# Performance work log

Hardware: AMD Instinct MI355X
Metric: run time of the kernel (lower is better)

The kernel has to match this reference:

```python
import jax, jax.numpy as jnp
import numpy as np
from jax import lax


def linear_recurrence(decays, impulses):
    """s[t] = decays[t]*s[t-1] + impulses[t], s[-1]=0, via associative scan over axis 0."""
    def comb(e1, e2):
        a1, b1 = e1
        a2, b2 = e2
        return a2 * a1, a2 * b1 + b2
    return lax.associative_scan(comb, (decays, impulses), axis=0)[1]


def setup_inputs() -> dict:
    key = jax.random.key(0)
    ks = jax.random.split(key, 6)
    b, T, d = 16, 1024, 128
    n, m, k = 64, 128, 16
    x = jax.random.normal(ks[0], (b, T, d), jnp.float32)
    R = jax.random.normal(ks[1], (d, k), jnp.float32)               # fixed projection
    theta = jax.random.uniform(ks[2], (k, n // 2), jnp.float32, -np.pi, np.pi)  # eig angles
    C = jax.random.uniform(ks[3], (k, m, n), jnp.float32, -1e-6, 1e-6) / n
    D = jax.random.uniform(ks[4], (k, m), jnp.float32, -1e-3, 1e-3)
    Do = jax.random.uniform(ks[5], (m,), jnp.float32, -1e-7, 1e-7)
    return {"x": x, "R": R, "theta": theta, "C": C, "D": D, "Do": Do}


def _ldstack(x, R, theta, C, D, Do, Delta=2, standard=True):
    c64 = jnp.complex64
    b, T, d = x.shape
    k, half = theta.shape
    n = 2 * half
    m = C.shape[1]
    # (b,T,d) -> (T,b,d) complex, project d -> k
    xc = jnp.transpose(x, (1, 0, 2)).astype(c64) @ R.astype(c64)  # (T,b,k)
    # unitary eigenvalues: lnλ = i*[θ, -θ]
    lnlam = (1j * jnp.concatenate([theta, -theta], axis=1)).astype(c64)  # (k,n)
    lam = jnp.exp(lnlam)
    # B' coefficients (log-space product over eigenvalue ratios, diag excluded)
    eye = jnp.eye(n, dtype=bool)
    ratios = jnp.where(eye[None], 0.0, lam[:, :, None] / lam[:, None, :])  # (k,n,n)
    B = jnp.exp(-jnp.sum(jnp.log(1.0 - ratios), axis=1))                    # (k,n)
    # C' coefficients: C'[k,j,m] = sum_i C[k,m,i] * λ[k,j]^{-(n-i)}
    powers = (n - jnp.arange(1, n + 1)).astype(c64)           # (n,) = [n-1,...,0]
    U = jnp.exp(-powers[None, :, None] * lnlam[:, None, :])   # (k,i,j)
    Cp = jnp.einsum('kmi,kij->kjm', C.astype(c64), U)         # (k,n,m)
    Dc = D.astype(c64)
    Doc = Do.astype(c64)

    alpha = None
    y = None
    for _ in range(Delta):
        Bx = (xc[..., None] * B).reshape(T, b, k * n)          # (T,b,k*n)
        if alpha is None:
            al = jnp.broadcast_to(lam.reshape(1, 1, k * n), (T, b, k * n))
        else:
            al = (alpha * lam).reshape(T, b, k * n)
        if standard:
            z = jnp.zeros((1, b, k * n), c64)
            al = jnp.concatenate([z, al[:-1]], axis=0)
            Bx = jnp.concatenate([z, Bx[:-1]], axis=0)
        s = linear_recurrence(al, Bx).reshape(T, b, k, n)      # (T,b,k,n)
        y = (jnp.einsum('tbkn,knm->tbkm', s, Cp)
             + xc[..., None] * Dc[None, None]
             + Doc)                                            # (T,b,k,m)
        ls = lam[None, None] * s
        alpha = (1.0 / jnp.sqrt(1.0 + jnp.abs(ls) ** 2)).astype(c64)  # recipsq
    y = jnp.mean(y, axis=2).real                               # (T,b,m)
    return jnp.transpose(y, (1, 0, 2))                         # (b,T,m)


def reference(x, R, theta, C, D, Do):
    return _ldstack(x, R, theta, C, D, Do, Delta=2, standard=True)
```

## Files before the change

### kernel.cpp

```cpp
#include <hip/hip_runtime.h>
#include <math.h>

#define TLEN 1024
#define BSZ  16
#define DIN  128
#define KP   16
#define NEIG 64
#define MOUT 128
#define CHUNK_T 256
#define NCHUNK  4

static constexpr size_t XCQ_OFF = 0;
static constexpr size_t LAM_OFF = 262144;
static constexpr size_t BQ_OFF  = 264192;
static constexpr size_t CP_OFF  = 266240;
static constexpr size_t ST_OFF  = 528384;
static constexpr size_t S2_OFF  = 593920;
static constexpr size_t P_OFF   = 8982528;

__device__ __forceinline__ float f32cos(float x) { return (float)cos((double)x); }
__device__ __forceinline__ float f32sin(float x) { return (float)sin((double)x); }

__device__ __forceinline__ float2 cdiv32(float ar, float ai, float cr, float ci) {
  float2 o;
  if (fabsf(ci) <= fabsf(cr)) {
    float rat = __fdiv_rn(ci, cr);
    float scl = __fdiv_rn(1.0f, __fadd_rn(cr, __fmul_rn(ci, rat)));
    o.x = __fmul_rn(__fadd_rn(ar, __fmul_rn(ai, rat)), scl);
    o.y = __fmul_rn(__fsub_rn(ai, __fmul_rn(ar, rat)), scl);
  } else {
    float rat = __fdiv_rn(cr, ci);
    float scl = __fdiv_rn(1.0f, __fadd_rn(ci, __fmul_rn(cr, rat)));
    o.x = __fmul_rn(__fadd_rn(__fmul_rn(ar, rat), ai), scl);
    o.y = __fmul_rn(__fsub_rn(__fmul_rn(ai, rat), ar), scl);
  }
  return o;
}

__global__ __launch_bounds__(256) void k_lam_B(const float* __restrict__ theta,
                        float2* __restrict__ lam, float2* __restrict__ Bq) {
  __shared__ float2 terms[4][64];
  int wid  = threadIdx.x >> 6;
  int lane = threadIdx.x & 63;
  int idx = blockIdx.x * 4 + wid;
  int k = idx >> 6, j = idx & 63;
  float thj = (j < 32) ? theta[k * 32 + j] : -theta[k * 32 + (j - 32)];
  float ljr = f32cos(thj), lji = f32sin(thj);
  float2 tm = make_float2(0.f, 0.f);
  if (lane != j) {
    int i = lane;
    float thi = (i < 32) ? theta[k * 32 + i] : -theta[k * 32 + (i - 32)];
    float lir = f32cos(thi), lii = f32sin(thi);
    float2 r = cdiv32(lir, lii, ljr, lji);
    float tr = __fsub_rn(1.0f, r.x);
    float ti = __fsub_rn(0.0f, r.y);
    double h = sqrt((double)tr * tr + (double)ti * ti);
    tm.x = (float)log(h);
    tm.y = (float)atan2((double)ti, (double)tr);
  }
  terms[wid][lane] = tm;
  __syncthreads();
  if (lane == 0) {
    lam[idx] = make_float2(ljr, lji);
    float sr = 0.f, si = 0.f;
    for (int i = 0; i < NEIG; ++i) {
      sr = __fadd_rn(sr, terms[wid][i].x);
      si = __fadd_rn(si, terms[wid][i].y);
    }
    float er = (float)exp((double)(-sr));
    float cc = f32cos(-si), ss = f32sin(-si);
    Bq[idx] = make_float2(__fmul_rn(er, cc), __fmul_rn(er, ss));
  }
}

__global__ __launch_bounds__(128) void k_Cp(const float* __restrict__ theta,
                     const float* __restrict__ C, float2* __restrict__ Cp) {
  __shared__ float2 sU[64];
  __shared__ float  sC[128][65];
  int tid = threadIdx.x;
  int kj = blockIdx.x;
  int j = kj & 63, k = kj >> 6;
  float lnim = (j < 32) ? theta[k * 32 + j] : -theta[k * 32 + (j - 32)];
  if (tid < 64) {
    int i = tid;
    float p = (float)(63 - i);
    float ph = -__fmul_rn(p, lnim);
    sU[i] = make_float2(f32cos(ph), f32sin(ph));
  }
  const float* Ck = C + ((size_t)k << 13);
  for (int e = tid; e < 128 * 64; e += 128) {
    sC[e >> 6][e & 63] = Ck[e];
  }
  __syncthreads();
  int m = tid;
  float ar = 0.f, ai = 0.f;
  #pragma unroll 8
  for (int i = 0; i < NEIG; ++i) {
    float Cv = sC[m][i];
    float2 U = sU[i];
    ar = __fadd_rn(ar, __fmul_rn(Cv, U.x));
    ai = __fadd_rn(ai, __fmul_rn(Cv, U.y));
  }
  Cp[(size_t)(k * 64 + j) * MOUT + m] = make_float2(ar, ai);
}

__global__ __launch_bounds__(256) void k_xc(const float* __restrict__ x,
                     const float* __restrict__ R, float* __restrict__ xcq) {
  __shared__ float sX[16][132];
  __shared__ float sR[128][16];
  int tid = threadIdx.x;
  int rBase = blockIdx.x * 16;
  for (int e = tid; e < DIN * KP; e += 256) sR[e >> 4][e & 15] = R[e];
  #pragma unroll
  for (int it = 0; it < 2; ++it) {
    int e = tid + it * 256;
    int row = e >> 5, q = e & 31;
    int g = rBase + row;
    int t = g >> 4, b = g & 15;
    float4 v = *(const float4*)(x + ((size_t)b * TLEN + t) * DIN + q * 4);
    *(float4*)&sX[row][q * 4] = v;
  }
  __syncthreads();
  int r = tid >> 4, k = tid & 15;
  double acc = 0.0;
  #pragma unroll 16
  for (int d = 0; d < DIN; ++d)
    acc = fma((double)sX[r][d], (double)sR[d][k], acc);
  xcq[(size_t)(rBase + r) * KP + k] = (float)acc;
}

__global__ __launch_bounds__(64) void k_scan(const float2* __restrict__ lam,
                        const float2* __restrict__ Bq,
                        const float* __restrict__ xcq,
                        float2* __restrict__ S2,
                        float* __restrict__ state, int c) {
  __shared__ float sXq[CHUNK_T];
  int j = threadIdx.x;
  int chain = blockIdx.x;
  int b = chain >> 4, k = chain & 15;
  int mode = k * 64 + j;
  int t0 = c * CHUNK_T;
  int tlBeg = (c == 0) ? 1 : 0;
  for (int i = j; i < CHUNK_T; i += 64) {
    int g = t0 + tlBeg - 1 + i;
    sXq[i] = xcq[(size_t)g * (BSZ * KP) + b * KP + k];
  }
  __syncthreads();
  float lr = lam[mode].x, li = lam[mode].y;
  float Br = Bq[mode].x,  Bi = Bq[mode].y;
  float* st = state + (size_t)(chain * 64 + j) * 4;
  float s1r, s1i, s2r, s2i;
  if (c == 0) { s1r = s1i = s2r = s2i = 0.f; }
  else        { s1r = st[0]; s1i = st[1]; s2r = st[2]; s2i = st[3]; }
  if (c == 0)
    S2[(size_t)(0 * BSZ + b) * 1024 + mode] = make_float2(s2r, s2i);

  int tl = tlBeg;
  for (; tl + 8 <= CHUNK_T; tl += 8) {
    float als[8];
    #pragma unroll
    for (int u = 0; u < 8; ++u) {
      float xq = sXq[tl - tlBeg + u];
      float lsr = __fsub_rn(__fmul_rn(lr, s1r), __fmul_rn(li, s1i));
      float lsi = __fadd_rn(__fmul_rn(lr, s1i), __fmul_rn(li, s1r));
      float h  = (float)sqrt((double)lsr * lsr + (double)lsi * lsi);
      als[u] = __fdiv_rn(1.0f, __fsqrt_rn(__fadd_rn(1.0f, __fmul_rn(h, h))));
      float bxr = __fmul_rn(xq, Br), bxi = __fmul_rn(xq, Bi);
      s1r = __fadd_rn(lsr, bxr);
      s1i = __fadd_rn(lsi, bxi);
    }
    #pragma unroll
    for (int u = 0; u < 8; ++u) {
      float xq = sXq[tl - tlBeg + u];
      float al = als[u];
      float bxr = __fmul_rn(xq, Br), bxi = __fmul_rn(xq, Bi);
      float a2r = __fmul_rn(al, lr), a2i = __fmul_rn(al, li);
      float t2r = __fsub_rn(__fmul_rn(a2r, s2r), __fmul_rn(a2i, s2i));
      float t2i = __fadd_rn(__fmul_rn(a2r, s2i), __fmul_rn(a2i, s2r));
      s2r = __fadd_rn(t2r, bxr);
      s2i = __fadd_rn(t2i, bxi);
      S2[(size_t)((tl + u) * BSZ + b) * 1024 + mode] = make_float2(s2r, s2i);
    }
  }
  for (; tl < CHUNK_T; ++tl) {
    float xq = sXq[tl - tlBeg];
    float lsr = __fsub_rn(__fmul_rn(lr, s1r), __fmul_rn(li, s1i));
    float lsi = __fadd_rn(__fmul_rn(lr, s1i), __fmul_rn(li, s1r));
    float h  = (float)sqrt((double)lsr * lsr + (double)lsi * lsi);
    float al = __fdiv_rn(1.0f, __fsqrt_rn(__fadd_rn(1.0f, __fmul_rn(h, h))));
    float bxr = __fmul_rn(xq, Br), bxi = __fmul_rn(xq, Bi);
    float a2r = __fmul_rn(al, lr), a2i = __fmul_rn(al, li);
    float t2r = __fsub_rn(__fmul_rn(a2r, s2r), __fmul_rn(a2i, s2i));
    float t2i = __fadd_rn(__fmul_rn(a2r, s2i), __fmul_rn(a2i, s2r));
    s2r = __fadd_rn(t2r, bxr);
    s2i = __fadd_rn(t2i, bxi);
    s1r = __fadd_rn(lsr, bxr);
    s1i = __fadd_rn(lsi, bxi);
    S2[(size_t)(tl * BSZ + b) * 1024 + mode] = make_float2(s2r, s2i);
  }
  st[0] = s1r; st[1] = s1i; st[2] = s2r; st[3] = s2i;
}

__global__ __launch_bounds__(256) void k_y(const float2* __restrict__ S2,
                     const float2* __restrict__ Cp, const float* __restrict__ xcq,
                     const float* __restrict__ D, const float* __restrict__ Dov,
                     float* __restrict__ P, int c) {
  __shared__ float2 sS2t[16][129];
  __shared__ float2 sCp[16][128];
  int tid = threadIdx.x;
  int kidx = blockIdx.x >> 5;
  int rt   = blockIdx.x & 31;
  int rowBase = rt * 128;
  int rg = tid & 15;
  int cg = tid >> 4;
  int c0 = cg * 8;
  float acc[8][8];
  #pragma unroll
  for (int jj = 0; jj < 8; ++jj)
    #pragma unroll
    for (int q = 0; q < 8; ++q) acc[jj][q] = 0.f;

  int a_n2[4], a_row[4], w_n[4], w_col2[4];
  #pragma unroll
  for (int it = 0; it < 4; ++it) {
    int e = tid + it * 256;
    a_n2[it] = (e & 7) * 2;  a_row[it] = e >> 3;
    w_n[it] = e >> 6;        w_col2[it] = (e & 63) * 2;
  }

  float4 regA[4], regB[4];
  #pragma unroll
  for (int it = 0; it < 4; ++it) {
    regA[it] = *(const float4*)(S2 + (size_t)(rowBase + a_row[it]) * 1024
                                   + kidx * 64 + a_n2[it]);
    regB[it] = *(const float4*)(Cp + (size_t)(kidx * 64 + w_n[it]) * MOUT + w_col2[it]);
  }

  #pragma unroll 1
  for (int nh = 0; nh < 4; ++nh) {
    __syncthreads();
    #pragma unroll
    for (int it = 0; it < 4; ++it) {
      sS2t[a_n2[it]][a_row[it]]     = make_float2(regA[it].x, regA[it].y);
      sS2t[a_n2[it] + 1][a_row[it]] = make_float2(regA[it].z, regA[it].w);
      *(float4*)&sCp[w_n[it]][w_col2[it]] = regB[it];
    }
    __syncthreads();
    if (nh < 3) {
      #pragma unroll
      for (int it = 0; it < 4; ++it) {
        regA[it] = *(const float4*)(S2 + (size_t)(rowBase + a_row[it]) * 1024
                                       + kidx * 64 + (nh + 1) * 16 + a_n2[it]);
        regB[it] = *(const float4*)(Cp + (size_t)(kidx * 64 + (nh + 1) * 16 + w_n[it]) * MOUT
                                       + w_col2[it]);
      }
    }
    #pragma unroll 4
    for (int n = 0; n < 16; ++n) {
      float2 a[8];
      #pragma unroll
      for (int jj = 0; jj < 8; ++jj) a[jj] = sS2t[n][rg + jj * 16];
      float4 w[4];
      #pragma unroll
      for (int q = 0; q < 4; ++q) w[q] = *(const float4*)&sCp[n][c0 + q * 2];
      float cx[8] = {w[0].x, w[0].z, w[1].x, w[1].z, w[2].x, w[2].z, w[3].x, w[3].z};
      float cy[8] = {w[0].y, w[0].w, w[1].y, w[1].w, w[2].y, w[2].w, w[3].y, w[3].w};
      #pragma unroll
      for (int jj = 0; jj < 8; ++jj)
        #pragma unroll
        for (int q = 0; q < 8; ++q)
          acc[jj][q] = __fadd_rn(acc[jj][q],
              __fsub_rn(__fmul_rn(a[jj].x, cx[q]), __fmul_rn(a[jj].y, cy[q])));
    }
  }
  float dv[8], ovv[8];
  *(float4*)&dv[0]  = *(const float4*)(D + kidx * MOUT + c0);
  *(float4*)&dv[4]  = *(const float4*)(D + kidx * MOUT + c0 + 4);
  *(float4*)&ovv[0] = *(const float4*)(Dov + c0);
  *(float4*)&ovv[4] = *(const float4*)(Dov + c0 + 4);
  #pragma unroll
  for (int jj = 0; jj < 8; ++jj) {
    int row = rowBase + rg + jj * 16;
    float xv = xcq[(size_t)(c * 4096 + row) * KP + kidx];
    float res[8];
    #pragma unroll
    for (int q = 0; q < 8; ++q)
      res[q] = __fadd_rn(__fadd_rn(acc[jj][q], __fmul_rn(xv, dv[q])), ovv[q]);
    float* pp = P + ((size_t)kidx * 4096 + row) * MOUT + c0;
    *(float4*)pp       = make_float4(res[0], res[1], res[2], res[3]);
    *(float4*)(pp + 4) = make_float4(res[4], res[5], res[6], res[7]);
  }
}

__global__ __launch_bounds__(256) void k_combine(const float* __restrict__ P,
                     float* __restrict__ out, int c) {
  int idx = blockIdx.x * 256 + threadIdx.x;
  int r  = idx >> 5;
  int m4 = (idx & 31) * 4;
  float4 s = *(const float4*)(P + (size_t)r * MOUT + m4);
  #pragma unroll
  for (int k = 1; k < KP; ++k) {
    float4 p = *(const float4*)(P + ((size_t)k * 4096 + r) * MOUT + m4);
    s.x = __fadd_rn(s.x, p.x);
    s.y = __fadd_rn(s.y, p.y);
    s.z = __fadd_rn(s.z, p.z);
    s.w = __fadd_rn(s.w, p.w);
  }
  int rg = c * 4096 + r;
  int t = rg >> 4, b = rg & 15;
  float4 res;
  res.x = __fdiv_rn(s.x, 16.0f);
  res.y = __fdiv_rn(s.y, 16.0f);
  res.z = __fdiv_rn(s.z, 16.0f);
  res.w = __fdiv_rn(s.w, 16.0f);
  *(float4*)(out + ((size_t)b * TLEN + t) * MOUT + m4) = res;
}

extern "C" void kernel_launch(void* const* d_in, const int* in_sizes, int n_in,
                              void* d_out, int out_size, void* d_ws, size_t ws_size,
                              hipStream_t stream) {
  const float* x     = (const float*)d_in[0];
  const float* R     = (const float*)d_in[1];
  const float* theta = (const float*)d_in[2];
  const float* C     = (const float*)d_in[3];
  const float* D     = (const float*)d_in[4];
  const float* Do    = (const float*)d_in[5];
  float* out = (float*)d_out;
  float* ws  = (float*)d_ws;
  float*  xcq = ws + XCQ_OFF;
  float2* lam = (float2*)(ws + LAM_OFF);
  float2* Bq  = (float2*)(ws + BQ_OFF);
  float2* Cp  = (float2*)(ws + CP_OFF);
  float*  st  = ws + ST_OFF;
  float2* S2  = (float2*)(ws + S2_OFF);
  float*  P   = ws + P_OFF;

  hipLaunchKernelGGL(k_lam_B, dim3(256),  dim3(256), 0, stream, theta, lam, Bq);
  hipLaunchKernelGGL(k_Cp,    dim3(1024), dim3(128), 0, stream, theta, C, Cp);
  hipLaunchKernelGGL(k_xc,    dim3(1024), dim3(256), 0, stream, x, R, xcq);
  for (int c = 0; c < NCHUNK; ++c) {
    hipLaunchKernelGGL(k_scan,    dim3(256), dim3(64),  0, stream, lam, Bq, xcq, S2, st, c);
    hipLaunchKernelGGL(k_y,       dim3(512), dim3(256), 0, stream, S2, Cp, xcq, D, Do, P, c);
    hipLaunchKernelGGL(k_combine, dim3(512), dim3(256), 0, stream, P, out, c);
  }
}
```

Baseline: 396.3 us.

## Halve k_y row tile to 64 and drop register prefetch to double block count

The k_y tile shrinks from 128 to 64 rows per block, so the grid doubles to 1024 blocks and each thread holds a 4x8 accumulator instead of 8x8. The register double-buffered prefetch of S2 and Cp tiles is removed in favour of direct global-to-shared loads inside the loop, and shared-memory padding is adjusted. The goal is more parallelism and occupancy on the device. In exchange, each loaded Cp tile is reused across fewer rows and global load latency is no longer overlapped with compute.

After: 372.1 us. -6.1%, faster.

```diff
diff --git a/kernel.cpp b/kernel.cpp
--- a/kernel.cpp
+++ b/kernel.cpp
@@ -205,68 +205,55 @@
                      const float2* __restrict__ Cp, const float* __restrict__ xcq,
                      const float* __restrict__ D, const float* __restrict__ Dov,
                      float* __restrict__ P, int c) {
-  __shared__ float2 sS2t[16][129];
-  __shared__ float2 sCp[16][128];
+  __shared__ float2 sS2t[16][65];
+  __shared__ float2 sCp[16][130];
   int tid = threadIdx.x;
-  int kidx = blockIdx.x >> 5;
-  int rt   = blockIdx.x & 31;
-  int rowBase = rt * 128;
+  int kidx = blockIdx.x >> 6;
+  int rt   = blockIdx.x & 63;
+  int rowBase = rt * 64;
   int rg = tid & 15;
   int cg = tid >> 4;
   int c0 = cg * 8;
-  float acc[8][8];
+  float acc[4][8];
   #pragma unroll
-  for (int jj = 0; jj < 8; ++jj)
+  for (int jj = 0; jj < 4; ++jj)
     #pragma unroll
     for (int q = 0; q < 8; ++q) acc[jj][q] = 0.f;
-
-  int a_n2[4], a_row[4], w_n[4], w_col2[4];
-  #pragma unroll
-  for (int it = 0; it < 4; ++it) {
-    int e = tid + it * 256;
-    a_n2[it] = (e & 7) * 2;  a_row[it] = e >> 3;
-    w_n[it] = e >> 6;        w_col2[it] = (e & 63) * 2;
-  }
-
-  float4 regA[4], regB[4];
-  #pragma unroll
-  for (int it = 0; it < 4; ++it) {
-    regA[it] = *(const float4*)(S2 + (size_t)(rowBase + a_row[it]) * 1024
-                                   + kidx * 64 + a_n2[it]);
-    regB[it] = *(const float4*)(Cp + (size_t)(kidx * 64 + w_n[it]) * MOUT + w_col2[it]);
-  }
 
   #pragma unroll 1
   for (int nh = 0; nh < 4; ++nh) {
     __syncthreads();
     #pragma unroll
+    for (int it = 0; it < 2; ++it) {
+      int e = tid + it * 256;
+      int n2 = (e & 7) * 2;
+      int row = e >> 3;
+      float4 v = *(const float4*)(S2 + (size_t)(rowBase + row) * 1024
+                                     + kidx * 64 + nh * 16 + n2);
+      sS2t[n2][row]     = make_float2(v.x, v.y);
+      sS2t[n2 + 1][row] = make_float2(v.z, v.w);
+    }
+    #pragma unroll
     for (int it = 0; it < 4; ++it) {
-      sS2t[a_n2[it]][a_row[it]]     = make_float2(regA[it].x, regA[it].y);
-      sS2t[a_n2[it] + 1][a_row[it]] = make_float2(regA[it].z, regA[it].w);
-      *(float4*)&sCp[w_n[it]][w_col2[it]] = regB[it];
+      int e = tid + it * 256;
+      int col2 = (e & 63) * 2;
+      int n = e >> 6;
+      float4 v = *(const float4*)(Cp + (size_t)(kidx * 64 + nh * 16 + n) * MOUT + col2);
+      *(float4*)&sCp[n][col2] = v;
     }
     __syncthreads();
-    if (nh < 3) {
-      #pragma unroll
-      for (int it = 0; it < 4; ++it) {
-        regA[it] = *(const float4*)(S2 + (size_t)(rowBase + a_row[it]) * 1024
-                                       + kidx * 64 + (nh + 1) * 16 + a_n2[it]);
-        regB[it] = *(const float4*)(Cp + (size_t)(kidx * 64 + (nh + 1) * 16 + w_n[it]) * MOUT
-                                       + w_col2[it]);
-      }
-    }
     #pragma unroll 4
     for (int n = 0; n < 16; ++n) {
-      float2 a[8];
+      float2 a[4];
       #pragma unroll
-      for (int jj = 0; jj < 8; ++jj) a[jj] = sS2t[n][rg + jj * 16];
+      for (int jj = 0; jj < 4; ++jj) a[jj] = sS2t[n][rg + jj * 16];
       float4 w[4];
       #pragma unroll
       for (int q = 0; q < 4; ++q) w[q] = *(const float4*)&sCp[n][c0 + q * 2];
       float cx[8] = {w[0].x, w[0].z, w[1].x, w[1].z, w[2].x, w[2].z, w[3].x, w[3].z};
       float cy[8] = {w[0].y, w[0].w, w[1].y, w[1].w, w[2].y, w[2].w, w[3].y, w[3].w};
       #pragma unroll
-      for (int jj = 0; jj < 8; ++jj)
+      for (int jj = 0; jj < 4; ++jj)
         #pragma unroll
         for (int q = 0; q < 8; ++q)
           acc[jj][q] = __fadd_rn(acc[jj][q],
@@ -279,7 +266,7 @@
   *(float4*)&ovv[0] = *(const float4*)(Dov + c0);
   *(float4*)&ovv[4] = *(const float4*)(Dov + c0 + 4);
   #pragma unroll
-  for (int jj = 0; jj < 8; ++jj) {
+  for (int jj = 0; jj < 4; ++jj) {
     int row = rowBase + rg + jj * 16;
     float xv = xcq[(size_t)(c * 4096 + row) * KP + kidx];
     float res[8];
@@ -339,8 +326,8 @@
   hipLaunchKernelGGL(k_Cp,    dim3(1024), dim3(128), 0, stream, theta, C, Cp);
   hipLaunchKernelGGL(k_xc,    dim3(1024), dim3(256), 0, stream, x, R, xcq);
   for (int c = 0; c < NCHUNK; ++c) {
-    hipLaunchKernelGGL(k_scan,    dim3(256), dim3(64),  0, stream, lam, Bq, xcq, S2, st, c);
-    hipLaunchKernelGGL(k_y,       dim3(512), dim3(256), 0, stream, S2, Cp, xcq, D, Do, P, c);
-    hipLaunchKernelGGL(k_combine, dim3(512), dim3(256), 0, stream, P, out, c);
-  }
-}
+    hipLaunchKernelGGL(k_scan,    dim3(256),  dim3(64),  0, stream, lam, Bq, xcq, S2, st, c);
+    hipLaunchKernelGGL(k_y,       dim3(1024), dim3(256), 0, stream, S2, Cp, xcq, D, Do, P, c);
+    hipLaunchKernelGGL(k_combine, dim3(512),  dim3(256), 0, stream, P, out, c);
+  }
+}
```
